# Performance work log

Measured on AMD Instinct MI355X. Metric: run time of the kernel, lower is better.

Reference implementation:

```python
import jax, jax.numpy as jnp
import numpy as np

B, N, D, H = 2, 2048, 1024, 16
HD = D // H
SCALING = HD ** -0.5
# fixed-point quant config (MASE integer quantizer): width=8, frac_width=5 for data/weight/bias
QW, QF = 8, 5


def quantize(x, width=QW, frac_width=QF):
    # MASE integer_quantizer: clamp(round(x * 2^f), -2^(w-1), 2^(w-1)-1) / 2^f
    scale = 2.0 ** frac_width
    xs = x * scale
    rounded = xs + jax.lax.stop_gradient(jnp.round(xs) - xs)  # STE round
    lo = -(2 ** (width - 1))
    hi = 2 ** (width - 1) - 1
    return jnp.clip(rounded, lo, hi) / scale


def linear_integer(x, W, b):
    # quantize activations, weights, bias; then fp matmul of dequantized values
    return quantize(x) @ quantize(W).T + quantize(b)


def bmm_integer(a, b):
    return jnp.einsum('bij,bjk->bik', quantize(a), quantize(b))


def _shape(t):
    # [B, N, D] -> [B*H, N, HD]
    return t.reshape(B, N, H, HD).transpose(0, 2, 1, 3).reshape(B * H, N, HD)


def setup_inputs() -> dict:
    key = jax.random.key(0)
    ks = jax.random.split(key, 9)
    w = lambda k: jax.random.normal(k, (D, D), jnp.float32) * 0.02
    bz = lambda k: jax.random.normal(k, (D,), jnp.float32) * 0.02
    return {
        'hidden_states': jax.random.normal(ks[0], (B, N, D), jnp.float32),
        'attention_mask': jnp.zeros((B, 1, N, N), jnp.float32),
        'q_w': w(ks[1]), 'q_b': bz(ks[2]),
        'k_w': w(ks[3]), 'k_b': bz(ks[4]),
        'v_w': w(ks[5]), 'v_b': bz(ks[6]),
        'o_w': w(ks[7]), 'o_b': bz(ks[8]),
    }


def reference(hidden_states, attention_mask, q_w, q_b, k_w, k_b, v_w, v_b, o_w, o_b):
    q = linear_integer(hidden_states, q_w, q_b) * SCALING          # [B,N,D]
    k = linear_integer(hidden_states, k_w, k_b)
    v = linear_integer(hidden_states, v_w, v_b)
    qh, kh, vh = _shape(q), _shape(k), _shape(v)                   # [B*H,N,HD]

    attn = bmm_integer(qh, kh.transpose(0, 2, 1))                  # [B*H,N,N]
    attn = attn.reshape(B, H, N, N) + attention_mask
    attn = jnp.maximum(attn, jnp.finfo(attn.dtype).min)
    attn = jax.nn.softmax(attn.reshape(B * H, N, N), axis=-1)

    ctx = bmm_integer(attn, vh)                                    # [B*H,N,HD]
    ctx = ctx.reshape(B, H, N, HD).transpose(0, 2, 1, 3).reshape(B, N, D)
    out = linear_integer(ctx, o_w, o_b)
    return out
```

## Files before the change

### kernel.cpp

```cpp
#include <hip/hip_runtime.h>
#include <cstdint>
#include <cfloat>
#include <climits>

#define NB 2
#define NN 2048
#define ND 1024
#define NH 16
#define NHD 64
#define NHB (NB*NH)
#define WS_NEEDED 25169920u

#if defined(__has_builtin)
#if __has_builtin(__builtin_amdgcn_sdot4)
#define HAS_SDOT4 1
#endif
#if __has_builtin(__builtin_amdgcn_exp2f)
#define EXP2F(x) __builtin_amdgcn_exp2f(x)
#else
#define EXP2F(x) exp2f(x)
#endif
#else
#define EXP2F(x) exp2f(x)
#endif

#define C2 0.0014088819735243784f

typedef __attribute__((ext_vector_type(4))) int int32x4;

__device__ __forceinline__ int dot4(int a, int b, int acc) {
#if defined(HAS_SDOT4)
  return __builtin_amdgcn_sdot4(a, b, acc, false);
#else
  acc += (int)(int8_t)(a & 255)       * (int)(int8_t)(b & 255);
  acc += (int)(int8_t)((a >> 8) & 255) * (int)(int8_t)((b >> 8) & 255);
  acc += (int)(int8_t)((a >> 16) & 255)* (int)(int8_t)((b >> 16) & 255);
  acc += (int)(int8_t)(a >> 24)        * (int)(int8_t)(b >> 24);
  return acc;
#endif
}

__device__ __forceinline__ int clampq(int v) {
  return min(127, max(-128, v));
}

__global__ __launch_bounds__(256) void zero_out_k(float4* __restrict__ out) {
  out[blockIdx.x * 256 + threadIdx.x] = float4{0.f, 0.f, 0.f, 0.f};
}

__device__ __forceinline__ int quant4(float4 f) {
  int a = clampq((int)rintf(f.x * 32.f));
  int b = clampq((int)rintf(f.y * 32.f));
  int c = clampq((int)rintf(f.z * 32.f));
  int d = clampq((int)rintf(f.w * 32.f));
  return (a & 255) | ((b & 255) << 8) | ((c & 255) << 16) | (d << 24);
}

__global__ __launch_bounds__(256) void quant_all_k(
    const float* __restrict__ hidden, const float* __restrict__ qw,
    const float* __restrict__ kw, const float* __restrict__ vw,
    const float* __restrict__ ow, const float* __restrict__ qb,
    const float* __restrict__ kb, const float* __restrict__ vb,
    const float* __restrict__ ob, int* __restrict__ xo, int* __restrict__ qwo,
    int* __restrict__ kwo, int* __restrict__ vwo, int* __restrict__ owo,
    int* __restrict__ qbo, int* __restrict__ kbo, int* __restrict__ vbo,
    int* __restrict__ obo) {
  const int bid = blockIdx.x;
  if (bid < 4096) {
    const int i = bid * 256 + threadIdx.x;
    xo[i] = quant4(reinterpret_cast<const float4*>(hidden)[i]);
  } else if (bid < 8192) {
    const int wb = bid - 4096;
    const int which = wb >> 10;
    const float* src = which == 0 ? qw : which == 1 ? kw : which == 2 ? vw : ow;
    int* dst = which == 0 ? qwo : which == 1 ? kwo : which == 2 ? vwo : owo;
    const int i = (wb & 1023) * 256 + threadIdx.x;
    dst[i] = quant4(reinterpret_cast<const float4*>(src)[i]);
  } else {
    const int which = bid - 8192;
    const float* src = which == 0 ? qb : which == 1 ? kb : which == 2 ? vb : ob;
    int* dst = which == 0 ? qbo : which == 1 ? kbo : which == 2 ? vbo : obo;
    const int i = threadIdx.x;
    dst[i] = quant4(reinterpret_cast<const float4*>(src)[i]);
  }
}

__global__ __launch_bounds__(256) void maskchk_k(const float* __restrict__ mask,
                                                 int* __restrict__ flags) {
  __shared__ int red[256];
  const int row = blockIdx.x;
  const int t = threadIdx.x;
  const float4* mr = (const float4*)(mask + (size_t)row * NN);
  int nz = 0;
#pragma unroll
  for (int i = 0; i < 2; ++i) {
    float4 f = mr[t * 2 + i];
    nz |= (f.x != 0.f) | (f.y != 0.f) | (f.z != 0.f) | (f.w != 0.f);
  }
  red[t] = nz;
  __syncthreads();
  for (int off = 128; off; off >>= 1) {
    if (t < off) red[t] |= red[t + off];
    __syncthreads();
  }
  if (t == 0) flags[row] = (red[0] == 0);
}

#define BM 64
#define BN 128
#define BK 64

template <bool OPROJ>
__device__ __forceinline__ void gemm_body(const int8_t* __restrict__ x,
                                          const int8_t* __restrict__ w,
                                          const int8_t* __restrict__ bq,
                                          int8_t* __restrict__ outq,
                                          float* __restrict__ outf,
                                          float scale) {
  __shared__ __align__(16) int8_t lA[2][BM * BK];
  __shared__ __align__(16) int8_t lB[2][BN * BK];
  const int t = threadIdx.x;
  const int wid = t >> 6;
  const int lane = t & 63;
  const int wr = wid >> 1, wc = wid & 1;
  const int bm = blockIdx.y * BM;
  const int bn = blockIdx.x * BN;

  const int srow = lane >> 2;
  const int scol = (lane & 3) * 16;
  const int frow = lane & 15;
  const int fk = (lane >> 4) * 16;

  const int8_t* gxa = x + (size_t)(bm + wid * 16 + srow) * ND + scol;
  const int8_t* gwb0 = w + (size_t)(bn + wid * 16 + srow) * ND + scol;
  const int8_t* gwb1 = w + (size_t)(bn + (wid + 4) * 16 + srow) * ND + scol;

#define STAGE(buf, ks)                                                          \
  do {                                                                          \
    const int k0_ = (ks) * BK;                                                  \
    __builtin_amdgcn_global_load_lds(                                           \
        (const __attribute__((address_space(1))) void*)(gxa + k0_),             \
        (__attribute__((address_space(3))) void*)(lA[buf] + wid * 1024), 16, 0, 0); \
    __builtin_amdgcn_global_load_lds(                                           \
        (const __attribute__((address_space(1))) void*)(gwb0 + k0_),            \
        (__attribute__((address_space(3))) void*)(lB[buf] + wid * 1024), 16, 0, 0); \
    __builtin_amdgcn_global_load_lds(                                           \
        (const __attribute__((address_space(1))) void*)(gwb1 + k0_),            \
        (__attribute__((address_space(3))) void*)(lB[buf] + (wid + 4) * 1024), 16, 0, 0); \
  } while (0)

  int32x4 acc[2][4];
#pragma unroll
  for (int i = 0; i < 2; ++i)
#pragma unroll
    for (int j = 0; j < 4; ++j) acc[i][j] = int32x4{0, 0, 0, 0};

  STAGE(0, 0);
  __syncthreads();

  for (int ks = 0; ks < ND / BK; ++ks) {
    const int cur = ks & 1;
    if (ks + 1 < ND / BK) STAGE(cur ^ 1, ks + 1);

    int32x4 af[2], bf[4];
#pragma unroll
    for (int mi = 0; mi < 2; ++mi)
      af[mi] = *(const int32x4*)(lA[cur] + (wr * 32 + mi * 16 + frow) * BK + fk);
#pragma unroll
    for (int ni = 0; ni < 4; ++ni)
      bf[ni] = *(const int32x4*)(lB[cur] + (wc * 64 + ni * 16 + frow) * BK + fk);
#pragma unroll
    for (int mi = 0; mi < 2; ++mi)
#pragma unroll
      for (int ni = 0; ni < 4; ++ni)
        acc[mi][ni] = __builtin_amdgcn_mfma_i32_16x16x64_i8(af[mi], bf[ni],
                                                            acc[mi][ni], 0, 0, 0);
    __syncthreads();
  }
#undef STAGE

  const int crow = (lane >> 4) * 4;
  const int ccol = lane & 15;
#pragma unroll
  for (int ni = 0; ni < 4; ++ni) {
    const int n = bn + wc * 64 + ni * 16 + ccol;
    const float bqf = (float)bq[n] * (1.f / 32.f);
    const int h = n >> 6, hd = n & 63;
#pragma unroll
    for (int mi = 0; mi < 2; ++mi) {
#pragma unroll
      for (int r = 0; r < 4; ++r) {
        const int m = bm + wr * 32 + mi * 16 + crow + r;
        const float val = (float)acc[mi][ni][r] * (1.f / 1024.f) + bqf;
        if (OPROJ) {
          outf[(size_t)m * ND + n] = val;
        } else {
          const int qv = clampq((int)rintf(val * scale * 32.f));
          const int b_ = m >> 11, nr = m & 2047;
          outq[(((size_t)((b_ << 4) + h) << 11) + nr) * NHD + hd] = (int8_t)qv;
        }
      }
    }
  }
}

__global__ __launch_bounds__(256) void gemm_qkv_k(const int8_t* __restrict__ x,
                                                  const int8_t* __restrict__ wq,
                                                  const int8_t* __restrict__ wk,
                                                  const int8_t* __restrict__ wv,
                                                  const int8_t* __restrict__ bqq,
                                                  const int8_t* __restrict__ bqk,
                                                  const int8_t* __restrict__ bqv,
                                                  int8_t* __restrict__ oq,
                                                  int8_t* __restrict__ ok,
                                                  int8_t* __restrict__ ov) {
  const int z = blockIdx.z;
  const int8_t* w = z == 0 ? wq : z == 1 ? wk : wv;
  const int8_t* bq = z == 0 ? bqq : z == 1 ? bqk : bqv;
  int8_t* out = z == 0 ? oq : z == 1 ? ok : ov;
  const float scale = z == 0 ? 0.125f : 1.0f;
  gemm_body<false>(x, w, bq, out, nullptr, scale);
}

__global__ __launch_bounds__(256) void gemm_o_k(const int8_t* __restrict__ x,
                                                const int8_t* __restrict__ w,
                                                const int8_t* __restrict__ bq,
                                                float* __restrict__ out) {
  gemm_body<true>(x, w, bq, nullptr, out, 1.0f);
}

__global__ __launch_bounds__(256) void attn_k(const int8_t* __restrict__ Q,
                                              const int8_t* __restrict__ K,
                                              const int8_t* __restrict__ V,
                                              const float* __restrict__ mask,
                                              const int* __restrict__ flags,
                                              int8_t* __restrict__ ctx) {
  __shared__ float wredf[4][32];
  __shared__ int wredi[4][32];
  __shared__ float sM[32];
  __shared__ int s_dirty[32];
  __shared__ int s_nm;
  __shared__ float sfb[NN];
  __shared__ float fred[256];
  __shared__ int ired[256];
  __shared__ int8_t pq[NN];

  const int t = threadIdx.x;
  const int hb = blockIdx.x, b = hb >> 4, h = hb & 15;
  const int q0 = blockIdx.y * 32;
  const int wid = t >> 6, lane = t & 63;
  const int l15 = lane & 15, l4 = lane >> 4;

  if (t == 0) s_nm = 1;
  __syncthreads();
  if (t < 32 && flags[b * NN + q0 + t] == 0) s_nm = 0;
  __syncthreads();
  const bool nomask = (s_nm != 0);

  const int8_t* Qh = Q + (size_t)hb * NN * NHD;
  const int8_t* Kh = K + (size_t)hb * NN * NHD;

  const int32x4 qb0 = *(const int32x4*)(Qh + (size_t)(q0 + l15) * NHD + l4 * 16);
  const int32x4 qb1 = *(const int32x4*)(Qh + (size_t)(q0 + 16 + l15) * NHD + l4 * 16);

  const float* mr0 = mask + ((size_t)(b * NN + q0 + l15)) * NN;
  const float* mr1 = mr0 + (size_t)16 * NN;
  const int kwbase = wid * 512;
  const int32x4 z4 = {0, 0, 0, 0};

  if (nomask) {
    int im0 = INT_MIN, im1 = INT_MIN;
    float s0 = 0.f, s1 = 0.f;
    for (int kt = 0; kt < 32; ++kt) {
      const int kb = kwbase + kt * 16;
      const int32x4 a = *(const int32x4*)(Kh + (size_t)(kb + l15) * NHD + l4 * 16);
      const int32x4 c0 = __builtin_amdgcn_mfma_i32_16x16x64_i8(a, qb0, z4, 0, 0, 0);
      const int32x4 c1 = __builtin_amdgcn_mfma_i32_16x16x64_i8(a, qb1, z4, 0, 0, 0);
#pragma unroll
      for (int r = 0; r < 4; ++r) {
        im0 = max(im0, c0[r]);
        s0 += EXP2F((float)c0[r] * C2);
        im1 = max(im1, c1[r]);
        s1 += EXP2F((float)c1[r] * C2);
      }
    }
#pragma unroll
    for (int off = 16; off <= 32; off <<= 1) {
      im0 = max(im0, __shfl_xor(im0, off)); s0 += __shfl_xor(s0, off);
      im1 = max(im1, __shfl_xor(im1, off)); s1 += __shfl_xor(s1, off);
    }
    if (lane < 16) { wredi[wid][lane] = im0; wredf[wid][lane] = s0; }
    else if (lane < 32) { wredi[wid][lane] = im1; wredf[wid][lane] = s1; }
    __syncthreads();
    if (t < 32) {
      int M = wredi[0][t];
      float S = wredf[0][t];
#pragma unroll
      for (int w2 = 1; w2 < 4; ++w2) {
        M = max(M, wredi[w2][t]);
        S += wredf[w2][t];
      }
      float lb = (M > 61440 || M < -61440) ? 0.f
                 : S * EXP2F(-(float)M * C2);
      s_dirty[t] = (lb >= 96.f) ? 0 : 1;
    }
    __syncthreads();
  } else {
    float m0 = -FLT_MAX, m1 = -FLT_MAX;
    for (int kt = 0; kt < 32; ++kt) {
      const int kb = kwbase + kt * 16;
      const int32x4 a = *(const int32x4*)(Kh + (size_t)(kb + l15) * NHD + l4 * 16);
      const int32x4 c0 = __builtin_amdgcn_mfma_i32_16x16x64_i8(a, qb0, z4, 0, 0, 0);
      const int32x4 c1 = __builtin_amdgcn_mfma_i32_16x16x64_i8(a, qb1, z4, 0, 0, 0);
      const int kofs = kb + l4 * 4;
#pragma unroll
      for (int r = 0; r < 4; ++r) {
        m0 = fmaxf(m0, fmaxf((float)c0[r] * (1.f / 1024.f) + mr0[kofs + r], -FLT_MAX));
        m1 = fmaxf(m1, fmaxf((float)c1[r] * (1.f / 1024.f) + mr1[kofs + r], -FLT_MAX));
      }
    }
#pragma unroll
    for (int off = 16; off <= 32; off <<= 1) {
      m0 = fmaxf(m0, __shfl_xor(m0, off));
      m1 = fmaxf(m1, __shfl_xor(m1, off));
    }
    if (lane < 16) wredf[wid][lane] = m0;
    else if (lane < 32) wredf[wid][lane] = m1;
    __syncthreads();
    if (t < 32) {
      float M = wredf[0][t];
#pragma unroll
      for (int w2 = 1; w2 < 4; ++w2) M = fmaxf(M, wredf[w2][t]);
      sM[t] = M;
    }
    __syncthreads();
    const float M0 = sM[l15], M1 = sM[16 + l15];
    float s0 = 0.f, s1 = 0.f;
    for (int kt = 0; kt < 32; ++kt) {
      const int kb = kwbase + kt * 16;
      const int32x4 a = *(const int32x4*)(Kh + (size_t)(kb + l15) * NHD + l4 * 16);
      const int32x4 c0 = __builtin_amdgcn_mfma_i32_16x16x64_i8(a, qb0, z4, 0, 0, 0);
      const int32x4 c1 = __builtin_amdgcn_mfma_i32_16x16x64_i8(a, qb1, z4, 0, 0, 0);
      const int kofs = kb + l4 * 4;
#pragma unroll
      for (int r = 0; r < 4; ++r) {
        float v0 = fmaxf((float)c0[r] * (1.f / 1024.f) + mr0[kofs + r], -FLT_MAX);
        float v1 = fmaxf((float)c1[r] * (1.f / 1024.f) + mr1[kofs + r], -FLT_MAX);
        s0 += __expf(v0 - M0);
        s1 += __expf(v1 - M1);
      }
    }
#pragma unroll
    for (int off = 16; off <= 32; off <<= 1) {
      s0 += __shfl_xor(s0, off);
      s1 += __shfl_xor(s1, off);
    }
    if (lane < 16) wredf[wid][lane] = s0;
    else if (lane < 32) wredf[wid][lane] = s1;
    __syncthreads();
    if (t < 32) {
      const float S = wredf[0][t] + wredf[1][t] + wredf[2][t] + wredf[3][t];
      s_dirty[t] = (S >= 96.f) ? 0 : 1;
    }
    __syncthreads();
  }

  {
    const int rl = t >> 3;
    if (!s_dirty[rl]) {
      int2* p = (int2*)(ctx + ((size_t)(b * NN + q0 + rl)) * ND + h * NHD);
      p[t & 7] = int2{0, 0};
    }
  }

  for (int rl = 0; rl < 32; ++rl) {
    if (!s_dirty[rl]) continue;
    __syncthreads();
    const int qrow = q0 + rl;
    const int* Qr = (const int*)(Qh + (size_t)qrow * NHD);
    const float* mrow = mask + ((size_t)(b * NN + qrow)) * NN;
    int qreg[16];
#pragma unroll
    for (int i = 0; i < 16; ++i) qreg[i] = Qr[i];
#pragma unroll
    for (int jj = 0; jj < 8; ++jj) {
      const int j = jj * 256 + t;
      const int* Kj = (const int*)(Kh + (size_t)j * NHD);
      int acc = 0;
#pragma unroll
      for (int i = 0; i < 16; ++i) acc = dot4(qreg[i], Kj[i], acc);
      sfb[j] = fmaxf((float)acc * (1.f / 1024.f) + mrow[j], -FLT_MAX);
    }
    __syncthreads();
    float lm = -INFINITY;
#pragma unroll
    for (int jj = 0; jj < 8; ++jj) lm = fmaxf(lm, sfb[jj * 256 + t]);
    fred[t] = lm;
    __syncthreads();
    for (int off = 128; off; off >>= 1) {
      if (t < off) fred[t] = fmaxf(fred[t], fred[t + off]);
      __syncthreads();
    }
    const float M = fred[0];
    __syncthreads();
    float ls = 0.f;
#pragma unroll
    for (int jj = 0; jj < 8; ++jj) {
      const int j = jj * 256 + t;
      const float e = expf(sfb[j] - M);
      sfb[j] = e; ls += e;
    }
    fred[t] = ls;
    __syncthreads();
    for (int off = 128; off; off >>= 1) {
      if (t < off) fred[t] += fred[t + off];
      __syncthreads();
    }
    const float S = fred[0];
#pragma unroll
    for (int jj = 0; jj < 8; ++jj) {
      const int j = jj * 256 + t;
      const int pi = (int)rintf(sfb[j] / S * 32.f);
      pq[j] = (int8_t)min(127, pi);
    }
    __syncthreads();
    const int8_t* Vh = V + (size_t)hb * NN * NHD;
    const int d = t & 63, ch = t >> 6;
    int a = 0;
    for (int j = ch * 512; j < ch * 512 + 512; ++j) {
      const int pv = pq[j];
      if (pv) a += pv * (int)Vh[(size_t)j * NHD + d];
    }
    ired[t] = a;
    __syncthreads();
    if (t < 64) {
      const int tot = ired[t] + ired[t + 64] + ired[t + 128] + ired[t + 192];
      ctx[((size_t)(b * NN + qrow)) * ND + h * NHD + t] =
          (int8_t)clampq((int)rintf((float)tot * (1.f / 32.f)));
    }
    __syncthreads();
  }
}

extern "C" void kernel_launch(void* const* d_in, const int* in_sizes, int n_in,
                              void* d_out, int out_size, void* d_ws, size_t ws_size,
                              hipStream_t stream) {
  float* out = (float*)d_out;

  if (ws_size < (size_t)WS_NEEDED) {
    zero_out_k<<<out_size / 1024, 256, 0, stream>>>((float4*)out);
    return;
  }

  const float* hidden = (const float*)d_in[0];
  const float* mask   = (const float*)d_in[1];
  const float* qw = (const float*)d_in[2];
  const float* qb = (const float*)d_in[3];
  const float* kw = (const float*)d_in[4];
  const float* kb = (const float*)d_in[5];
  const float* vw = (const float*)d_in[6];
  const float* vb = (const float*)d_in[7];
  const float* ow = (const float*)d_in[8];
  const float* ob = (const float*)d_in[9];

  char* ws = (char*)d_ws;
  int8_t* x_i8  = (int8_t*)(ws + 0);
  int8_t* qw_i8 = (int8_t*)(ws + 4194304);
  int8_t* kw_i8 = (int8_t*)(ws + 5242880);
  int8_t* vw_i8 = (int8_t*)(ws + 6291456);
  int8_t* ow_i8 = (int8_t*)(ws + 7340032);
  int8_t* qb_i8 = (int8_t*)(ws + 8388608);
  int8_t* kb_i8 = (int8_t*)(ws + 8389632);
  int8_t* vb_i8 = (int8_t*)(ws + 8390656);
  int8_t* ob_i8 = (int8_t*)(ws + 8391680);
  int8_t* Q_i8  = (int8_t*)(ws + 8392704);
  int8_t* K_i8  = (int8_t*)(ws + 12587008);
  int8_t* V_i8  = (int8_t*)(ws + 16781312);
  int8_t* c_i8  = (int8_t*)(ws + 20975616);
  int* mflags   = (int*)(ws + 0);

  quant_all_k<<<8196, 256, 0, stream>>>(hidden, qw, kw, vw, ow, qb, kb, vb, ob,
                                        (int*)x_i8, (int*)qw_i8, (int*)kw_i8,
                                        (int*)vw_i8, (int*)ow_i8, (int*)qb_i8,
                                        (int*)kb_i8, (int*)vb_i8, (int*)ob_i8);

  gemm_qkv_k<<<dim3(ND / BN, NB * NN / BM, 3), 256, 0, stream>>>(
      x_i8, qw_i8, kw_i8, vw_i8, qb_i8, kb_i8, vb_i8, Q_i8, K_i8, V_i8);

  maskchk_k<<<NB * NN, 256, 0, stream>>>(mask, mflags);

  attn_k<<<dim3(NHB, NN / 32), 256, 0, stream>>>(Q_i8, K_i8, V_i8, mask, mflags, c_i8);

  gemm_o_k<<<dim3(ND / BN, NB * NN / BM), 256, 0, stream>>>(c_i8, ow_i8, ob_i8, out);
}
```

Baseline: 184.2 us.

## Process 64 query rows per attention block and fuse mask check into quant kernel

```diff
diff --git a/kernel.cpp b/kernel.cpp
--- a/kernel.cpp
+++ b/kernel.cpp
@@ -9,7 +9,7 @@
 #define NH 16
 #define NHD 64
 #define NHB (NB*NH)
-#define WS_NEEDED 25169920u
+#define WS_NEEDED 25186304u
 
 #if defined(__has_builtin)
 #if __has_builtin(__builtin_amdgcn_sdot4)
@@ -61,49 +61,46 @@
     const float* __restrict__ kw, const float* __restrict__ vw,
     const float* __restrict__ ow, const float* __restrict__ qb,
     const float* __restrict__ kb, const float* __restrict__ vb,
-    const float* __restrict__ ob, int* __restrict__ xo, int* __restrict__ qwo,
-    int* __restrict__ kwo, int* __restrict__ vwo, int* __restrict__ owo,
-    int* __restrict__ qbo, int* __restrict__ kbo, int* __restrict__ vbo,
-    int* __restrict__ obo) {
+    const float* __restrict__ ob, const float* __restrict__ mask,
+    int* __restrict__ xo, int* __restrict__ qwo, int* __restrict__ kwo,
+    int* __restrict__ vwo, int* __restrict__ owo, int* __restrict__ qbo,
+    int* __restrict__ kbo, int* __restrict__ vbo, int* __restrict__ obo,
+    int* __restrict__ flags) {
+  __shared__ int red[256];
   const int bid = blockIdx.x;
+  const int t = threadIdx.x;
   if (bid < 4096) {
-    const int i = bid * 256 + threadIdx.x;
+    const int i = bid * 256 + t;
     xo[i] = quant4(reinterpret_cast<const float4*>(hidden)[i]);
   } else if (bid < 8192) {
     const int wb = bid - 4096;
     const int which = wb >> 10;
     const float* src = which == 0 ? qw : which == 1 ? kw : which == 2 ? vw : ow;
     int* dst = which == 0 ? qwo : which == 1 ? kwo : which == 2 ? vwo : owo;
-    const int i = (wb & 1023) * 256 + threadIdx.x;
+    const int i = (wb & 1023) * 256 + t;
     dst[i] = quant4(reinterpret_cast<const float4*>(src)[i]);
-  } else {
+  } else if (bid < 8196) {
     const int which = bid - 8192;
     const float* src = which == 0 ? qb : which == 1 ? kb : which == 2 ? vb : ob;
     int* dst = which == 0 ? qbo : which == 1 ? kbo : which == 2 ? vbo : obo;
-    const int i = threadIdx.x;
-    dst[i] = quant4(reinterpret_cast<const float4*>(src)[i]);
-  }
-}
-
-__global__ __launch_bounds__(256) void maskchk_k(const float* __restrict__ mask,
-                                                 int* __restrict__ flags) {
-  __shared__ int red[256];
-  const int row = blockIdx.x;
-  const int t = threadIdx.x;
-  const float4* mr = (const float4*)(mask + (size_t)row * NN);
-  int nz = 0;
-#pragma unroll
-  for (int i = 0; i < 2; ++i) {
-    float4 f = mr[t * 2 + i];
-    nz |= (f.x != 0.f) | (f.y != 0.f) | (f.z != 0.f) | (f.w != 0.f);
-  }
-  red[t] = nz;
-  __syncthreads();
-  for (int off = 128; off; off >>= 1) {
-    if (t < off) red[t] |= red[t + off];
-    __syncthreads();
-  }
-  if (t == 0) flags[row] = (red[0] == 0);
+    dst[t] = quant4(reinterpret_cast<const float4*>(src)[t]);
+  } else {
+    const int row = bid - 8196;
+    const float4* mr = (const float4*)(mask + (size_t)row * NN);
+    int nz = 0;
+#pragma unroll
+    for (int i = 0; i < 2; ++i) {
+      float4 f = mr[t * 2 + i];
+      nz |= (f.x != 0.f) | (f.y != 0.f) | (f.z != 0.f) | (f.w != 0.f);
+    }
+    red[t] = nz;
+    __syncthreads();
+    for (int off = 128; off; off >>= 1) {
+      if (t < off) red[t] |= red[t + off];
+      __syncthreads();
+    }
+    if (t == 0) flags[row] = (red[0] == 0);
+  }
 }
 
 #define BM 64
@@ -235,10 +232,10 @@
                                               const float* __restrict__ mask,
                                               const int* __restrict__ flags,
                                               int8_t* __restrict__ ctx) {
-  __shared__ float wredf[4][32];
-  __shared__ int wredi[4][32];
-  __shared__ float sM[32];
-  __shared__ int s_dirty[32];
+  __shared__ float wredf[4][64];
+  __shared__ int wredi[4][64];
+  __shared__ float sM[64];
+  __shared__ int s_dirty[64];
   __shared__ int s_nm;
   __shared__ float sfb[NN];
   __shared__ float fred[256];
@@ -247,52 +244,75 @@
 
   const int t = threadIdx.x;
   const int hb = blockIdx.x, b = hb >> 4, h = hb & 15;
-  const int q0 = blockIdx.y * 32;
+  const int q0 = blockIdx.y * 64;
   const int wid = t >> 6, lane = t & 63;
   const int l15 = lane & 15, l4 = lane >> 4;
 
   if (t == 0) s_nm = 1;
   __syncthreads();
-  if (t < 32 && flags[b * NN + q0 + t] == 0) s_nm = 0;
+  if (t < 64 && flags[b * NN + q0 + t] == 0) s_nm = 0;
   __syncthreads();
   const bool nomask = (s_nm != 0);
 
   const int8_t* Qh = Q + (size_t)hb * NN * NHD;
   const int8_t* Kh = K + (size_t)hb * NN * NHD;
 
-  const int32x4 qb0 = *(const int32x4*)(Qh + (size_t)(q0 + l15) * NHD + l4 * 16);
-  const int32x4 qb1 = *(const int32x4*)(Qh + (size_t)(q0 + 16 + l15) * NHD + l4 * 16);
+  int32x4 qf0 = *(const int32x4*)(Qh + (size_t)(q0 + l15) * NHD + l4 * 16);
+  int32x4 qf1 = *(const int32x4*)(Qh + (size_t)(q0 + 16 + l15) * NHD + l4 * 16);
+  int32x4 qf2 = *(const int32x4*)(Qh + (size_t)(q0 + 32 + l15) * NHD + l4 * 16);
+  int32x4 qf3 = *(const int32x4*)(Qh + (size_t)(q0 + 48 + l15) * NHD + l4 * 16);
 
   const float* mr0 = mask + ((size_t)(b * NN + q0 + l15)) * NN;
   const float* mr1 = mr0 + (size_t)16 * NN;
+  const float* mr2 = mr0 + (size_t)32 * NN;
+  const float* mr3 = mr0 + (size_t)48 * NN;
   const int kwbase = wid * 512;
   const int32x4 z4 = {0, 0, 0, 0};
 
+#define KFRAG(kt) (*(const int32x4*)(Kh + (size_t)(kwbase + (kt) * 16 + l15) * NHD + l4 * 16))
+
   if (nomask) {
-    int im0 = INT_MIN, im1 = INT_MIN;
-    float s0 = 0.f, s1 = 0.f;
+    int im0 = INT_MIN, im1 = INT_MIN, im2 = INT_MIN, im3 = INT_MIN;
+    float sa0 = 0.f, sb0 = 0.f, sa1 = 0.f, sb1 = 0.f;
+    float sa2 = 0.f, sb2 = 0.f, sa3 = 0.f, sb3 = 0.f;
+    int32x4 a = KFRAG(0);
     for (int kt = 0; kt < 32; ++kt) {
-      const int kb = kwbase + kt * 16;
-      const int32x4 a = *(const int32x4*)(Kh + (size_t)(kb + l15) * NHD + l4 * 16);
-      const int32x4 c0 = __builtin_amdgcn_mfma_i32_16x16x64_i8(a, qb0, z4, 0, 0, 0);
-      const int32x4 c1 = __builtin_amdgcn_mfma_i32_16x16x64_i8(a, qb1, z4, 0, 0, 0);
+      const int32x4 an = KFRAG(kt == 31 ? 31 : kt + 1);
+      const int32x4 c0 = __builtin_amdgcn_mfma_i32_16x16x64_i8(a, qf0, z4, 0, 0, 0);
+      const int32x4 c1 = __builtin_amdgcn_mfma_i32_16x16x64_i8(a, qf1, z4, 0, 0, 0);
+      const int32x4 c2 = __builtin_amdgcn_mfma_i32_16x16x64_i8(a, qf2, z4, 0, 0, 0);
+      const int32x4 c3 = __builtin_amdgcn_mfma_i32_16x16x64_i8(a, qf3, z4, 0, 0, 0);
 #pragma unroll
       for (int r = 0; r < 4; ++r) {
-        im0 = max(im0, c0[r]);
-        s0 += EXP2F((float)c0[r] * C2);
-        im1 = max(im1, c1[r]);
-        s1 += EXP2F((float)c1[r] * C2);
+        im0 = max(im0, c0[r]); im1 = max(im1, c1[r]);
+        im2 = max(im2, c2[r]); im3 = max(im3, c3[r]);
       }
-    }
+      sa0 += EXP2F((float)c0[0] * C2) + EXP2F((float)c0[1] * C2);
+      sb0 += EXP2F((float)c0[2] * C2) + EXP2F((float)c0[3] * C2);
+      sa1 += EXP2F((float)c1[0] * C2) + EXP2F((float)c1[1] * C2);
+      sb1 += EXP2F((float)c1[2] * C2) + EXP2F((float)c1[3] * C2);
+      sa2 += EXP2F((float)c2[0] * C2) + EXP2F((float)c2[1] * C2);
+      sb2 += EXP2F((float)c2[2] * C2) + EXP2F((float)c2[3] * C2);
+      sa3 += EXP2F((float)c3[0] * C2) + EXP2F((float)c3[1] * C2);
+      sb3 += EXP2F((float)c3[2] * C2) + EXP2F((float)c3[3] * C2);
+      a = an;
+    }
+    float s0 = sa0 + sb0, s1 = sa1 + sb1, s2 = sa2 + sb2, s3 = sa3 + sb3;
 #pragma unroll
     for (int off = 16; off <= 32; off <<= 1) {
       im0 = max(im0, __shfl_xor(im0, off)); s0 += __shfl_xor(s0, off);
       im1 = max(im1, __shfl_xor(im1, off)); s1 += __shfl_xor(s1, off);
-    }
-    if (lane < 16) { wredi[wid][lane] = im0; wredf[wid][lane] = s0; }
-    else if (lane < 32) { wredi[wid][lane] = im1; wredf[wid][lane] = s1; }
-    __syncthreads();
-    if (t < 32) {
+      im2 = max(im2, __shfl_xor(im2, off)); s2 += __shfl_xor(s2, off);
+      im3 = max(im3, __shfl_xor(im3, off)); s3 += __shfl_xor(s3, off);
+    }
+    if (lane < 16) {
+      wredi[wid][lane] = im0;      wredf[wid][lane] = s0;
+      wredi[wid][16 + lane] = im1; wredf[wid][16 + lane] = s1;
+      wredi[wid][32 + lane] = im2; wredf[wid][32 + lane] = s2;
+      wredi[wid][48 + lane] = im3; wredf[wid][48 + lane] = s3;
+    }
+    __syncthreads();
+    if (t < 64) {
       int M = wredi[0][t];
       float S = wredf[0][t];
 #pragma unroll
@@ -300,34 +320,40 @@
         M = max(M, wredi[w2][t]);
         S += wredf[w2][t];
       }
-      float lb = (M > 61440 || M < -61440) ? 0.f
-                 : S * EXP2F(-(float)M * C2);
+      float lb = (M > 61440 || M < -61440) ? 0.f : S * EXP2F(-(float)M * C2);
       s_dirty[t] = (lb >= 96.f) ? 0 : 1;
     }
     __syncthreads();
   } else {
-    float m0 = -FLT_MAX, m1 = -FLT_MAX;
+    float m0 = -FLT_MAX, m1 = -FLT_MAX, m2 = -FLT_MAX, m3 = -FLT_MAX;
     for (int kt = 0; kt < 32; ++kt) {
-      const int kb = kwbase + kt * 16;
-      const int32x4 a = *(const int32x4*)(Kh + (size_t)(kb + l15) * NHD + l4 * 16);
-      const int32x4 c0 = __builtin_amdgcn_mfma_i32_16x16x64_i8(a, qb0, z4, 0, 0, 0);
-      const int32x4 c1 = __builtin_amdgcn_mfma_i32_16x16x64_i8(a, qb1, z4, 0, 0, 0);
-      const int kofs = kb + l4 * 4;
+      const int32x4 a = KFRAG(kt);
+      const int32x4 c0 = __builtin_amdgcn_mfma_i32_16x16x64_i8(a, qf0, z4, 0, 0, 0);
+      const int32x4 c1 = __builtin_amdgcn_mfma_i32_16x16x64_i8(a, qf1, z4, 0, 0, 0);
+      const int32x4 c2 = __builtin_amdgcn_mfma_i32_16x16x64_i8(a, qf2, z4, 0, 0, 0);
+      const int32x4 c3 = __builtin_amdgcn_mfma_i32_16x16x64_i8(a, qf3, z4, 0, 0, 0);
+      const int kofs = kwbase + kt * 16 + l4 * 4;
 #pragma unroll
       for (int r = 0; r < 4; ++r) {
         m0 = fmaxf(m0, fmaxf((float)c0[r] * (1.f / 1024.f) + mr0[kofs + r], -FLT_MAX));
         m1 = fmaxf(m1, fmaxf((float)c1[r] * (1.f / 1024.f) + mr1[kofs + r], -FLT_MAX));
+        m2 = fmaxf(m2, fmaxf((float)c2[r] * (1.f / 1024.f) + mr2[kofs + r], -FLT_MAX));
+        m3 = fmaxf(m3, fmaxf((float)c3[r] * (1.f / 1024.f) + mr3[kofs + r], -FLT_MAX));
       }
     }
 #pragma unroll
     for (int off = 16; off <= 32; off <<= 1) {
       m0 = fmaxf(m0, __shfl_xor(m0, off));
       m1 = fmaxf(m1, __shfl_xor(m1, off));
-    }
-    if (lane < 16) wredf[wid][lane] = m0;
-    else if (lane < 32) wredf[wid][lane] = m1;
-    __syncthreads();
-    if (t < 32) {
+      m2 = fmaxf(m2, __shfl_xor(m2, off));
+      m3 = fmaxf(m3, __shfl_xor(m3, off));
+    }
+    if (lane < 16) {
+      wredf[wid][lane] = m0;      wredf[wid][16 + lane] = m1;
+      wredf[wid][32 + lane] = m2; wredf[wid][48 + lane] = m3;
+    }
+    __syncthreads();
+    if (t < 64) {
       float M = wredf[0][t];
 #pragma unroll
       for (int w2 = 1; w2 < 4; ++w2) M = fmaxf(M, wredf[w2][t]);
@@ -335,45 +361,52 @@
     }
     __syncthreads();
     const float M0 = sM[l15], M1 = sM[16 + l15];
-    float s0 = 0.f, s1 = 0.f;
+    const float M2 = sM[32 + l15], M3 = sM[48 + l15];
+    float s0 = 0.f, s1 = 0.f, s2 = 0.f, s3 = 0.f;
     for (int kt = 0; kt < 32; ++kt) {
-      const int kb = kwbase + kt * 16;
-      const int32x4 a = *(const int32x4*)(Kh + (size_t)(kb + l15) * NHD + l4 * 16);
-      const int32x4 c0 = __builtin_amdgcn_mfma_i32_16x16x64_i8(a, qb0, z4, 0, 0, 0);
-      const int32x4 c1 = __builtin_amdgcn_mfma_i32_16x16x64_i8(a, qb1, z4, 0, 0, 0);
-      const int kofs = kb + l4 * 4;
+      const int32x4 a = KFRAG(kt);
+      const int32x4 c0 = __builtin_amdgcn_mfma_i32_16x16x64_i8(a, qf0, z4, 0, 0, 0);
+      const int32x4 c1 = __builtin_amdgcn_mfma_i32_16x16x64_i8(a, qf1, z4, 0, 0, 0);
+      const int32x4 c2 = __builtin_amdgcn_mfma_i32_16x16x64_i8(a, qf2, z4, 0, 0, 0);
+      const int32x4 c3 = __builtin_amdgcn_mfma_i32_16x16x64_i8(a, qf3, z4, 0, 0, 0);
+      const int kofs = kwbase + kt * 16 + l4 * 4;
 #pragma unroll
       for (int r = 0; r < 4; ++r) {
-        float v0 = fmaxf((float)c0[r] * (1.f / 1024.f) + mr0[kofs + r], -FLT_MAX);
-        float v1 = fmaxf((float)c1[r] * (1.f / 1024.f) + mr1[kofs + r], -FLT_MAX);
-        s0 += __expf(v0 - M0);
-        s1 += __expf(v1 - M1);
+        s0 += __expf(fmaxf((float)c0[r] * (1.f / 1024.f) + mr0[kofs + r], -FLT_MAX) - M0);
+        s1 += __expf(fmaxf((float)c1[r] * (1.f / 1024.f) + mr1[kofs + r], -FLT_MAX) - M1);
+        s2 += __expf(fmaxf((float)c2[r] * (1.f / 1024.f) + mr2[kofs + r], -FLT_MAX) - M2);
+        s3 += __expf(fmaxf((float)c3[r] * (1.f / 1024.f) + mr3[kofs + r], -FLT_MAX) - M3);
       }
     }
 #pragma unroll
     for (int off = 16; off <= 32; off <<= 1) {
-      s0 += __shfl_xor(s0, off);
-      s1 += __shfl_xor(s1, off);
-    }
-    if (lane < 16) wredf[wid][lane] = s0;
-    else if (lane < 32) wredf[wid][lane] = s1;
-    __syncthreads();
-    if (t < 32) {
+      s0 += __shfl_xor(s0, off); s1 += __shfl_xor(s1, off);
+      s2 += __shfl_xor(s2, off); s3 += __shfl_xor(s3, off);
+    }
+    if (lane < 16) {
+      wredf[wid][lane] = s0;      wredf[wid][16 + lane] = s1;
+      wredf[wid][32 + lane] = s2; wredf[wid][48 + lane] = s3;
+    }
+    __syncthreads();
+    if (t < 64) {
       const float S = wredf[0][t] + wredf[1][t] + wredf[2][t] + wredf[3][t];
       s_dirty[t] = (S >= 96.f) ? 0 : 1;
     }
     __syncthreads();
   }
+#undef KFRAG
 
   {
-    const int rl = t >> 3;
+    const int rl = t >> 2;
     if (!s_dirty[rl]) {
-      int2* p = (int2*)(ctx + ((size_t)(b * NN + q0 + rl)) * ND + h * NHD);
-      p[t & 7] = int2{0, 0};
-    }
-  }
-
-  for (int rl = 0; rl < 32; ++rl) {
+      int4* p = (int4*)(ctx + ((size_t)(b * NN + q0 + rl)) * ND + h * NHD);
+      const int4 z = {0, 0, 0, 0};
+      p[(t & 3) * 2] = z;
+      p[(t & 3) * 2 + 1] = z;
+    }
+  }
+
+  for (int rl = 0; rl < 64; ++rl) {
     if (!s_dirty[rl]) continue;
     __syncthreads();
     const int qrow = q0 + rl;
@@ -477,19 +510,18 @@
   int8_t* K_i8  = (int8_t*)(ws + 12587008);
   int8_t* V_i8  = (int8_t*)(ws + 16781312);
   int8_t* c_i8  = (int8_t*)(ws + 20975616);
-  int* mflags   = (int*)(ws + 0);
-
-  quant_all_k<<<8196, 256, 0, stream>>>(hidden, qw, kw, vw, ow, qb, kb, vb, ob,
-                                        (int*)x_i8, (int*)qw_i8, (int*)kw_i8,
-                                        (int*)vw_i8, (int*)ow_i8, (int*)qb_i8,
-                                        (int*)kb_i8, (int*)vb_i8, (int*)ob_i8);
+  int* mflags   = (int*)(ws + 25169920);
+
+  quant_all_k<<<12292, 256, 0, stream>>>(hidden, qw, kw, vw, ow, qb, kb, vb, ob,
+                                         mask, (int*)x_i8, (int*)qw_i8,
+                                         (int*)kw_i8, (int*)vw_i8, (int*)ow_i8,
+                                         (int*)qb_i8, (int*)kb_i8, (int*)vb_i8,
+                                         (int*)ob_i8, mflags);
 
   gemm_qkv_k<<<dim3(ND / BN, NB * NN / BM, 3), 256, 0, stream>>>(
       x_i8, qw_i8, kw_i8, vw_i8, qb_i8, kb_i8, vb_i8, Q_i8, K_i8, V_i8);
 
-  maskchk_k<<<NB * NN, 256, 0, stream>>>(mask, mflags);
-
-  attn_k<<<dim3(NHB, NN / 32), 256, 0, stream>>>(Q_i8, K_i8, V_i8, mask, mflags, c_i8);
+  attn_k<<<dim3(NHB, NN / 64), 256, 0, stream>>>(Q_i8, K_i8, V_i8, mask, mflags, c_i8);
 
   gemm_o_k<<<dim3(ND / BN, NB * NN / BM), 256, 0, stream>>>(c_i8, ow_i8, ob_i8, out);
 }
```

Result: no change. 183.8 us (-0.2%).
